# Performance work log

Hardware: AMD Instinct MI355X
Metric: run time of the kernel (lower is better)

Reference implementation:

```python
import jax, jax.numpy as jnp
import numpy as np

CLIP_LEN = 8      # == num_frame
NUM_NODES = 7     # == group_size
NUM_BASIC = 1024
NUM_MIXED = 8192
T = 2 * CLIP_LEN - 1          # 15 temporal offsets
N = 1 + NUM_NODES * CLIP_LEN  # 57 graph size


def setup_inputs() -> dict:
    key = jax.random.key(0)
    k1, k2, k3, k4 = jax.random.split(key, 4)
    mat = jax.random.normal(k1, (NUM_BASIC, NUM_NODES, NUM_NODES), dtype=jnp.float32)
    temp_extent = jax.random.normal(k2, (NUM_BASIC, T), dtype=jnp.float32)
    # nn.Linear(num_basic, num_mixed): weight [out,in], bias [out]
    W = jax.random.normal(k3, (NUM_MIXED, NUM_BASIC), dtype=jnp.float32) * (1.0 / np.sqrt(NUM_BASIC))
    b = jax.random.normal(k4, (NUM_MIXED,), dtype=jnp.float32) * 0.01
    return {"mat": mat, "temp_extent": temp_extent, "W": W, "b": b}


def reference(mat, temp_extent, W, b):
    n, cl = NUM_NODES, CLIP_LEN
    Hb = mat.shape[0]
    te = jax.nn.sigmoid(temp_extent) + 1.0                      # [Hb, T]
    x = jnp.einsum('ht,hnm->htmn', te, mat)                     # [Hb, T, n, n]
    x = jax.nn.relu(x)
    x = jnp.transpose(x, (1, 2, 3, 0)).reshape(T * n, n, Hb)    # (t m) n h
    y = x @ W.T + b                                             # [(t m), n, Hm]
    y = jax.nn.relu(jnp.transpose(y, (2, 1, 0)))                # [Hm, n, T*n]
    Hm = y.shape[0]
    # vectorized version of the per-frame slice-write loop:
    # frame i reads cols n*(cl-1-i) : n*(2*cl-1-i) of y
    starts = n * (cl - 1 - jnp.arange(cl))                      # [cl]
    idx = starts[:, None] + jnp.arange(n * cl)[None, :]         # [cl, n*cl]
    blocks = y[:, :, idx]                                       # [Hm, n, cl, n*cl]
    blocks = jnp.transpose(blocks, (0, 2, 1, 3)).reshape(Hm, n * cl, n * cl)
    base = jnp.zeros((Hm, N, N), dtype=y.dtype)
    base = base.at[:, 0::7, 0::7].set(1.0)                      # person-node anchors
    mixed = base.at[:, 1:, 1:].set(blocks)                      # [Hm, N, N]
    # degree normalization D^{-1/2} A D^{-1/2} (row sums, clamped at 1)
    d = jnp.clip(mixed.sum(axis=2), 1.0, None) ** -0.5          # [Hm, N]
    ret = d[:, :, None] * mixed * d[:, None, :]
    return ret
```

## Files before the change

kernel.cpp:

```cpp
#include <hip/hip_runtime.h>

#define HB 1024
#define HM 8192
#define NR 735
#define NPAD 768
#define NOUT 57

#define BM 64
#define BN 128
#define BK 64

typedef __attribute__((ext_vector_type(8))) _Float16 half8;
typedef __attribute__((ext_vector_type(4))) _Float16 half4v;
typedef __attribute__((ext_vector_type(4))) float floatx4;

__global__ __launch_bounds__(256) void prep_kernel(
    const float* __restrict__ mat, const float* __restrict__ tex,
    const float4* __restrict__ W,
    _Float16* __restrict__ Xh, half4v* __restrict__ Wh) {
  const int blk = blockIdx.x;
  if (blk < NPAD) {
    const int r = blk;
    const int n = r % 7;
    const int tm = r / 7;
    const int m = tm % 7;
    const int t = tm / 7;
#pragma unroll
    for (int i = 0; i < 4; ++i) {
      const int h = i * 256 + threadIdx.x;
      float v = 0.f;
      if (r < NR) {
        const float mv = mat[h * 49 + n * 7 + m];
        const float te = 1.f / (1.f + expf(-tex[h * 15 + t])) + 1.f;
        v = te * mv;
        v = v > 0.f ? v : 0.f;
      }
      Xh[r * HB + h] = (_Float16)v;
    }
  } else {
    const int idx = (blk - NPAD) * 256 + threadIdx.x;
    const float4 v = W[idx];
    half4v h;
    h.x = (_Float16)v.x;
    h.y = (_Float16)v.y;
    h.z = (_Float16)v.z;
    h.w = (_Float16)v.w;
    Wh[idx] = h;
  }
}

#define STAGE(pp, k0)                                                          \
  do {                                                                         \
    _Pragma("unroll")                                                          \
    for (int it_ = 0; it_ < 2; ++it_) {                                        \
      const int c_ = wave * 2 + it_;                                           \
      const int row_ = ((c_ & 3) * 16) + srow;                                 \
      const int kof_ = ((c_ >> 2) * 32) + skh;                                 \
      __builtin_amdgcn_global_load_lds(                                        \
          (const __attribute__((address_space(1))) void*)(                     \
              A + abase + (size_t)row_ * HB + (k0) + kof_),                    \
          (__attribute__((address_space(3))) void*)(&As[pp][c_ * 512 + lane * 8]), \
          16, 0, 0);                                                           \
    }                                                                          \
    _Pragma("unroll")                                                          \
    for (int it_ = 0; it_ < 4; ++it_) {                                        \
      const int c_ = wave * 4 + it_;                                           \
      const int row_ = ((c_ & 7) * 16) + srow;                                 \
      const int kof_ = ((c_ >> 3) * 32) + skh;                                 \
      __builtin_amdgcn_global_load_lds(                                        \
          (const __attribute__((address_space(1))) void*)(                     \
              B + bbase + (size_t)row_ * HB + (k0) + kof_),                    \
          (__attribute__((address_space(3))) void*)(&Bs[pp][c_ * 512 + lane * 8]), \
          16, 0, 0);                                                           \
    }                                                                          \
  } while (0)

__global__ __launch_bounds__(256) void gemm_kernel(
    const _Float16* __restrict__ A,
    const _Float16* __restrict__ B,
    const float* __restrict__ bias,
    float* __restrict__ Y) {
  __shared__ __align__(16) _Float16 As[2][BM * BK];
  __shared__ __align__(16) _Float16 Bs[2][BN * BK];

  const int tid = threadIdx.x;
  const int lane = tid & 63;
  const int wave = tid >> 6;

  const int bid = blockIdx.x;
  const int wg = (bid & 7) * 96 + (bid >> 3);
  const int bn = wg % 6;
  const int bm = wg / 6;

  const int wm = (wave >> 1) * 32;
  const int wn = (wave & 1) * 64;

  floatx4 acc[2][4] = {};

  const int srow = lane >> 2;
  const int skh = (lane & 3) * 8;
  const size_t abase = (size_t)(bm * BM) * HB;
  const size_t bbase = (size_t)(bn * BN) * HB;

  const int mrow = lane & 15;
  const int quad = lane >> 4;

  STAGE(0, 0);
  __syncthreads();

  int p = 0;
  for (int k0 = 0; k0 < HB; k0 += BK) {
    if (k0 + BK < HB) STAGE(p ^ 1, k0 + BK);

    half8 af[2][2], bf[2][4];
#pragma unroll
    for (int s = 0; s < 2; ++s) {
#pragma unroll
      for (int i = 0; i < 2; ++i)
        af[s][i] =
            *(const half8*)(&As[p][s * 2048 + (wm + i * 16 + mrow) * 32 + quad * 8]);
#pragma unroll
      for (int j = 0; j < 4; ++j)
        bf[s][j] =
            *(const half8*)(&Bs[p][s * 4096 + (wn + j * 16 + mrow) * 32 + quad * 8]);
    }
#pragma unroll
    for (int s = 0; s < 2; ++s)
#pragma unroll
      for (int i = 0; i < 2; ++i)
#pragma unroll
        for (int j = 0; j < 4; ++j)
          acc[i][j] = __builtin_amdgcn_mfma_f32_16x16x32_f16(af[s][i], bf[s][j],
                                                             acc[i][j], 0, 0, 0);

    __syncthreads();
    p ^= 1;
  }

#pragma unroll
  for (int i = 0; i < 2; ++i) {
#pragma unroll
    for (int j = 0; j < 4; ++j) {
#pragma unroll
      for (int reg = 0; reg < 4; ++reg) {
        const int grow = bm * BM + wm + i * 16 + quad * 4 + reg;
        const int gcol = bn * BN + wn + j * 16 + mrow;
        float v = acc[i][j][reg] + bias[grow];
        v = v > 0.f ? v : 0.f;
        Y[(size_t)grow * NPAD + gcol] = v;
      }
    }
  }
}

__global__ __launch_bounds__(256) void epilogue_kernel(
    const float* __restrict__ Y, float* __restrict__ out) {
  const int j0 = blockIdx.x * 4;
  __shared__ float ly[4][NR];
  __shared__ float dd[4][NOUT];

#pragma unroll
  for (int jj = 0; jj < 4; ++jj)
    for (int i = threadIdx.x; i < NR; i += 256)
      ly[jj][i] = Y[(size_t)(j0 + jj) * NPAD + i];
  __syncthreads();

  if (threadIdx.x < 4 * NOUT) {
    const int jj = threadIdx.x / NOUT;
    const int r = threadIdx.x % NOUT;
    float s;
    if (r == 0) {
      s = 9.f;
    } else {
      const int c = (r - 1) / 7;
      const int n = (r - 1) % 7;
      const int base = 7 * (7 - c);
      s = (n == 6) ? 1.f : 0.f;
      const float* lyj = ly[jj];
#pragma unroll
      for (int q = 0; q < 56; ++q) s += lyj[(base + q) * 7 + n];
    }
    s = s < 1.f ? 1.f : s;
    dd[jj][r] = rsqrtf(s);
  }
  __syncthreads();

  float4* ob = (float4*)(out + (size_t)j0 * (NOUT * NOUT));
  for (int v4 = threadIdx.x; v4 < NOUT * NOUT; v4 += 256) {
    float4 o;
#pragma unroll
    for (int e = 0; e < 4; ++e) {
      const int f = v4 * 4 + e;
      const int jj = f / (NOUT * NOUT);
      const int rem = f - jj * (NOUT * NOUT);
      const int r = rem / NOUT;
      const int q = rem - r * NOUT;
      const float* lyj = ly[jj];
      const float* dj = dd[jj];
      float val;
      if (r == 0) {
        val = (q % 7 == 0) ? dj[0] * dj[q] : 0.f;
      } else {
        const int c = (r - 1) / 7;
        const int n = (r - 1) % 7;
        if (q == 0)
          val = (n == 6) ? dj[r] * dj[0] : 0.f;
        else
          val = dj[r] * lyj[(7 * (7 - c) + q - 1) * 7 + n] * dj[q];
      }
      (&o.x)[e] = val;
    }
    ob[v4] = o;
  }
}

extern "C" void kernel_launch(void* const* d_in, const int* in_sizes, int n_in,
                              void* d_out, int out_size, void* d_ws, size_t ws_size,
                              hipStream_t stream) {
  const float* mat = (const float*)d_in[0];
  const float* tex = (const float*)d_in[1];
  const float* W = (const float*)d_in[2];
  const float* b = (const float*)d_in[3];
  float* out = (float*)d_out;

  char* ws = (char*)d_ws;
  _Float16* Xh = (_Float16*)(ws);
  _Float16* Wh = (_Float16*)(ws + (size_t)NPAD * HB * 2);
  float* Y = (float*)(ws + (size_t)NPAD * HB * 2 + (size_t)HM * HB * 2);

  prep_kernel<<<NPAD + HM * HB / 4 / 256, 256, 0, stream>>>(
      mat, tex, (const float4*)W, Xh, (half4v*)Wh);
  gemm_kernel<<<HM / BM * (NPAD / BN), 256, 0, stream>>>(Wh, Xh, b, Y);
  epilogue_kernel<<<HM / 4, 256, 0, stream>>>(Y, out);
}
```

Measured before the change: 187.1 us.

## Load GEMM fragments directly from global into registers, dropping LDS staging

The GEMM main loop no longer stages A and B tiles through LDS with global_load_lds and barriers. Each wave now reads its MFMA fragments straight from global memory into registers, using a two-set register double buffer that loads the next k-slice while the current one is multiplied. This removes the LDS traffic and __syncthreads, in exchange for redundant global/L2 reads, since waves sharing rows or columns each fetch their own copy. The last iteration issues a harmless wrap-around prefetch at k=0.

```diff
diff --git a/kernel.cpp b/kernel.cpp
--- a/kernel.cpp
+++ b/kernel.cpp
@@ -8,7 +8,6 @@
 
 #define BM 64
 #define BN 128
-#define BK 64
 
 typedef __attribute__((ext_vector_type(8))) _Float16 half8;
 typedef __attribute__((ext_vector_type(4))) _Float16 half4v;
@@ -49,30 +48,31 @@
   }
 }
 
-#define STAGE(pp, k0)                                                          \
-  do {                                                                         \
-    _Pragma("unroll")                                                          \
-    for (int it_ = 0; it_ < 2; ++it_) {                                        \
-      const int c_ = wave * 2 + it_;                                           \
-      const int row_ = ((c_ & 3) * 16) + srow;                                 \
-      const int kof_ = ((c_ >> 2) * 32) + skh;                                 \
-      __builtin_amdgcn_global_load_lds(                                        \
-          (const __attribute__((address_space(1))) void*)(                     \
-              A + abase + (size_t)row_ * HB + (k0) + kof_),                    \
-          (__attribute__((address_space(3))) void*)(&As[pp][c_ * 512 + lane * 8]), \
-          16, 0, 0);                                                           \
-    }                                                                          \
-    _Pragma("unroll")                                                          \
-    for (int it_ = 0; it_ < 4; ++it_) {                                        \
-      const int c_ = wave * 4 + it_;                                           \
-      const int row_ = ((c_ & 7) * 16) + srow;                                 \
-      const int kof_ = ((c_ >> 3) * 32) + skh;                                 \
-      __builtin_amdgcn_global_load_lds(                                        \
-          (const __attribute__((address_space(1))) void*)(                     \
-              B + bbase + (size_t)row_ * HB + (k0) + kof_),                    \
-          (__attribute__((address_space(3))) void*)(&Bs[pp][c_ * 512 + lane * 8]), \
-          16, 0, 0);                                                           \
-    }                                                                          \
+#define LOADF(af, bf, k0)                                                     \
+  do {                                                                        \
+    _Pragma("unroll")                                                         \
+    for (int s_ = 0; s_ < 2; ++s_) {                                          \
+      _Pragma("unroll")                                                       \
+      for (int i_ = 0; i_ < 2; ++i_)                                          \
+        af[s_][i_] =                                                          \
+            *(const half8*)(Abase + (size_t)i_ * 16 * HB + (k0) + s_ * 32);   \
+      _Pragma("unroll")                                                       \
+      for (int j_ = 0; j_ < 4; ++j_)                                          \
+        bf[s_][j_] =                                                          \
+            *(const half8*)(Bbase + (size_t)j_ * 16 * HB + (k0) + s_ * 32);   \
+    }                                                                         \
+  } while (0)
+
+#define MFMAS(af, bf)                                                         \
+  do {                                                                        \
+    _Pragma("unroll")                                                         \
+    for (int s_ = 0; s_ < 2; ++s_)                                            \
+      _Pragma("unroll")                                                       \
+      for (int i_ = 0; i_ < 2; ++i_)                                          \
+        _Pragma("unroll")                                                     \
+        for (int j_ = 0; j_ < 4; ++j_)                                        \
+          acc[i_][j_] = __builtin_amdgcn_mfma_f32_16x16x32_f16(               \
+              af[s_][i_], bf[s_][j_], acc[i_][j_], 0, 0, 0);                  \
   } while (0)
 
 __global__ __launch_bounds__(256) void gemm_kernel(
@@ -80,9 +80,6 @@
     const _Float16* __restrict__ B,
     const float* __restrict__ bias,
     float* __restrict__ Y) {
-  __shared__ __align__(16) _Float16 As[2][BM * BK];
-  __shared__ __align__(16) _Float16 Bs[2][BN * BK];
-
   const int tid = threadIdx.x;
   const int lane = tid & 63;
   const int wave = tid >> 6;
@@ -95,46 +92,23 @@
   const int wm = (wave >> 1) * 32;
   const int wn = (wave & 1) * 64;
 
-  floatx4 acc[2][4] = {};
-
-  const int srow = lane >> 2;
-  const int skh = (lane & 3) * 8;
-  const size_t abase = (size_t)(bm * BM) * HB;
-  const size_t bbase = (size_t)(bn * BN) * HB;
-
   const int mrow = lane & 15;
   const int quad = lane >> 4;
 
-  STAGE(0, 0);
-  __syncthreads();
-
-  int p = 0;
-  for (int k0 = 0; k0 < HB; k0 += BK) {
-    if (k0 + BK < HB) STAGE(p ^ 1, k0 + BK);
-
-    half8 af[2][2], bf[2][4];
-#pragma unroll
-    for (int s = 0; s < 2; ++s) {
-#pragma unroll
-      for (int i = 0; i < 2; ++i)
-        af[s][i] =
-            *(const half8*)(&As[p][s * 2048 + (wm + i * 16 + mrow) * 32 + quad * 8]);
-#pragma unroll
-      for (int j = 0; j < 4; ++j)
-        bf[s][j] =
-            *(const half8*)(&Bs[p][s * 4096 + (wn + j * 16 + mrow) * 32 + quad * 8]);
-    }
-#pragma unroll
-    for (int s = 0; s < 2; ++s)
-#pragma unroll
-      for (int i = 0; i < 2; ++i)
-#pragma unroll
-        for (int j = 0; j < 4; ++j)
-          acc[i][j] = __builtin_amdgcn_mfma_f32_16x16x32_f16(af[s][i], bf[s][j],
-                                                             acc[i][j], 0, 0, 0);
-
-    __syncthreads();
-    p ^= 1;
+  const _Float16* Abase = A + (size_t)(bm * BM + wm + mrow) * HB + quad * 8;
+  const _Float16* Bbase = B + (size_t)(bn * BN + wn + mrow) * HB + quad * 8;
+
+  floatx4 acc[2][4] = {};
+  half8 a0[2][2], b0[2][4], a1[2][2], b1[2][4];
+
+  LOADF(a0, b0, 0);
+#pragma unroll 1
+  for (int k0 = 0; k0 < HB; k0 += 128) {
+    LOADF(a1, b1, k0 + 64);
+    MFMAS(a0, b0);
+    const int kn = (k0 + 128 < HB) ? k0 + 128 : 0;
+    LOADF(a0, b0, kn);
+    MFMAS(a1, b1);
   }
 
 #pragma unroll
```

Result: slower. 234.2 us (+25.2%).

## Fuse fp32-to-fp16 weight conversion into GEMM A-tile loading

Applied to the files above, without the earlier changes.

Drops the separate pass that converted the full weight matrix to fp16 in the workspace. The GEMM now reads fp32 weights directly through registers, converts them, and writes them to LDS while the MFMAs for the current tile run. BK is halved to 32 to keep the register-staged A path and the LDS footprint manageable. This saves a full write and re-read of the 16 MB fp16 weight copy. The cost is that each of the 6 column blocks re-reads the fp32 weights at twice the bytes, and the K loop runs twice as many iterations with more barriers.

```diff
diff --git a/kernel.cpp b/kernel.cpp
--- a/kernel.cpp
+++ b/kernel.cpp
@@ -8,75 +8,57 @@
 
 #define BM 64
 #define BN 128
-#define BK 64
+#define BK 32
 
 typedef __attribute__((ext_vector_type(8))) _Float16 half8;
-typedef __attribute__((ext_vector_type(4))) _Float16 half4v;
 typedef __attribute__((ext_vector_type(4))) float floatx4;
 
 __global__ __launch_bounds__(256) void prep_kernel(
     const float* __restrict__ mat, const float* __restrict__ tex,
-    const float4* __restrict__ W,
-    _Float16* __restrict__ Xh, half4v* __restrict__ Wh) {
-  const int blk = blockIdx.x;
-  if (blk < NPAD) {
-    const int r = blk;
-    const int n = r % 7;
-    const int tm = r / 7;
-    const int m = tm % 7;
-    const int t = tm / 7;
-#pragma unroll
-    for (int i = 0; i < 4; ++i) {
-      const int h = i * 256 + threadIdx.x;
-      float v = 0.f;
-      if (r < NR) {
-        const float mv = mat[h * 49 + n * 7 + m];
-        const float te = 1.f / (1.f + expf(-tex[h * 15 + t])) + 1.f;
-        v = te * mv;
-        v = v > 0.f ? v : 0.f;
-      }
-      Xh[r * HB + h] = (_Float16)v;
-    }
-  } else {
-    const int idx = (blk - NPAD) * 256 + threadIdx.x;
-    const float4 v = W[idx];
-    half4v h;
-    h.x = (_Float16)v.x;
-    h.y = (_Float16)v.y;
-    h.z = (_Float16)v.z;
-    h.w = (_Float16)v.w;
-    Wh[idx] = h;
-  }
-}
-
-#define STAGE(pp, k0)                                                          \
+    _Float16* __restrict__ Xh) {
+  const int r = blockIdx.x;
+  const int n = r % 7;
+  const int tm = r / 7;
+  const int m = tm % 7;
+  const int t = tm / 7;
+#pragma unroll
+  for (int i = 0; i < 4; ++i) {
+    const int h = i * 256 + threadIdx.x;
+    float v = 0.f;
+    if (r < NR) {
+      const float mv = mat[h * 49 + n * 7 + m];
+      const float te = 1.f / (1.f + expf(-tex[h * 15 + t])) + 1.f;
+      v = te * mv;
+      v = v > 0.f ? v : 0.f;
+    }
+    Xh[r * HB + h] = (_Float16)v;
+  }
+}
+
+#define STAGE_B(pp, k0)                                                        \
   do {                                                                         \
     _Pragma("unroll")                                                          \
     for (int it_ = 0; it_ < 2; ++it_) {                                        \
       const int c_ = wave * 2 + it_;                                           \
-      const int row_ = ((c_ & 3) * 16) + srow;                                 \
-      const int kof_ = ((c_ >> 2) * 32) + skh;                                 \
+      const int row_ = c_ * 16 + srow;                                         \
       __builtin_amdgcn_global_load_lds(                                        \
           (const __attribute__((address_space(1))) void*)(                     \
-              A + abase + (size_t)row_ * HB + (k0) + kof_),                    \
-          (__attribute__((address_space(3))) void*)(&As[pp][c_ * 512 + lane * 8]), \
-          16, 0, 0);                                                           \
-    }                                                                          \
-    _Pragma("unroll")                                                          \
-    for (int it_ = 0; it_ < 4; ++it_) {                                        \
-      const int c_ = wave * 4 + it_;                                           \
-      const int row_ = ((c_ & 7) * 16) + srow;                                 \
-      const int kof_ = ((c_ >> 3) * 32) + skh;                                 \
-      __builtin_amdgcn_global_load_lds(                                        \
-          (const __attribute__((address_space(1))) void*)(                     \
-              B + bbase + (size_t)row_ * HB + (k0) + kof_),                    \
-          (__attribute__((address_space(3))) void*)(&Bs[pp][c_ * 512 + lane * 8]), \
+              B + bbase + (size_t)row_ * HB + (k0) + skh),                     \
+          (__attribute__((address_space(3))) void*)(&Bs[pp][c_ * 512]),        \
           16, 0, 0);                                                           \
     }                                                                          \
   } while (0)
 
+#define CVT8(h, r0, r1)                                                        \
+  do {                                                                         \
+    h[0] = (_Float16)r0.x; h[1] = (_Float16)r0.y;                              \
+    h[2] = (_Float16)r0.z; h[3] = (_Float16)r0.w;                              \
+    h[4] = (_Float16)r1.x; h[5] = (_Float16)r1.y;                              \
+    h[6] = (_Float16)r1.z; h[7] = (_Float16)r1.w;                              \
+  } while (0)
+
 __global__ __launch_bounds__(256) void gemm_kernel(
-    const _Float16* __restrict__ A,
+    const float* __restrict__ W,
     const _Float16* __restrict__ B,
     const float* __restrict__ bias,
     float* __restrict__ Y) {
@@ -97,42 +79,57 @@
 
   floatx4 acc[2][4] = {};
 
+  const int arow = wave * 16 + (lane >> 2);
+  const int akh = (lane & 3) * 8;
+  const float* Ap = W + (size_t)(bm * BM + arow) * HB + akh;
+  const int alds = arow * BK + akh;
+
   const int srow = lane >> 2;
   const int skh = (lane & 3) * 8;
-  const size_t abase = (size_t)(bm * BM) * HB;
   const size_t bbase = (size_t)(bn * BN) * HB;
 
   const int mrow = lane & 15;
   const int quad = lane >> 4;
 
-  STAGE(0, 0);
+  {
+    float4 r0 = *(const float4*)(Ap + 0);
+    float4 r1 = *(const float4*)(Ap + 4);
+    half8 h;
+    CVT8(h, r0, r1);
+    *(half8*)(&As[0][alds]) = h;
+  }
+  STAGE_B(0, 0);
   __syncthreads();
 
   int p = 0;
   for (int k0 = 0; k0 < HB; k0 += BK) {
-    if (k0 + BK < HB) STAGE(p ^ 1, k0 + BK);
-
-    half8 af[2][2], bf[2][4];
-#pragma unroll
-    for (int s = 0; s < 2; ++s) {
-#pragma unroll
-      for (int i = 0; i < 2; ++i)
-        af[s][i] =
-            *(const half8*)(&As[p][s * 2048 + (wm + i * 16 + mrow) * 32 + quad * 8]);
+    const int next = k0 + BK;
+    float4 r0, r1;
+    if (next < HB) {
+      r0 = *(const float4*)(Ap + next);
+      r1 = *(const float4*)(Ap + next + 4);
+      STAGE_B(p ^ 1, next);
+    }
+
+    half8 af[2], bf[4];
+#pragma unroll
+    for (int i = 0; i < 2; ++i)
+      af[i] = *(const half8*)(&As[p][(wm + i * 16 + mrow) * BK + quad * 8]);
+#pragma unroll
+    for (int j = 0; j < 4; ++j)
+      bf[j] = *(const half8*)(&Bs[p][(wn + j * 16 + mrow) * BK + quad * 8]);
+#pragma unroll
+    for (int i = 0; i < 2; ++i)
 #pragma unroll
       for (int j = 0; j < 4; ++j)
-        bf[s][j] =
-            *(const half8*)(&Bs[p][s * 4096 + (wn + j * 16 + mrow) * 32 + quad * 8]);
-    }
-#pragma unroll
-    for (int s = 0; s < 2; ++s)
-#pragma unroll
-      for (int i = 0; i < 2; ++i)
-#pragma unroll
-        for (int j = 0; j < 4; ++j)
-          acc[i][j] = __builtin_amdgcn_mfma_f32_16x16x32_f16(af[s][i], bf[s][j],
-                                                             acc[i][j], 0, 0, 0);
-
+        acc[i][j] =
+            __builtin_amdgcn_mfma_f32_16x16x32_f16(af[i], bf[j], acc[i][j], 0, 0, 0);
+
+    if (next < HB) {
+      half8 h;
+      CVT8(h, r0, r1);
+      *(half8*)(&As[p ^ 1][alds]) = h;
+    }
     __syncthreads();
     p ^= 1;
   }
@@ -225,11 +222,9 @@
 
   char* ws = (char*)d_ws;
   _Float16* Xh = (_Float16*)(ws);
-  _Float16* Wh = (_Float16*)(ws + (size_t)NPAD * HB * 2);
-  float* Y = (float*)(ws + (size_t)NPAD * HB * 2 + (size_t)HM * HB * 2);
-
-  prep_kernel<<<NPAD + HM * HB / 4 / 256, 256, 0, stream>>>(
-      mat, tex, (const float4*)W, Xh, (half4v*)Wh);
-  gemm_kernel<<<HM / BM * (NPAD / BN), 256, 0, stream>>>(Wh, Xh, b, Y);
+  float* Y = (float*)(ws + (size_t)NPAD * HB * 2);
+
+  prep_kernel<<<NPAD, 256, 0, stream>>>(mat, tex, Xh);
+  gemm_kernel<<<HM / BM * (NPAD / BN), 256, 0, stream>>>(W, Xh, b, Y);
   epilogue_kernel<<<HM / 4, 256, 0, stream>>>(Y, out);
 }
```

Measured after the change: 196.9 us. +5.3%, slower.

## Triple-buffer GEMM LDS stages with BK 32 and one barrier per step

Applied to the files above, without the earlier changes.

The GEMM K-tile shrinks from 64 to 32 and the two LDS buffers become three. Loads run two stages ahead, and each iteration waits with vmcnt so that only the current stage must have landed. A single raw s_barrier per iteration replaces the trailing __syncthreads, so global-to-LDS loads can overlap MFMA work across iterations. In exchange there are twice as many loop iterations and fewer MFMAs per barrier, and correctness depends on hand-counted vmcnt values.

```diff
diff --git a/kernel.cpp b/kernel.cpp
--- a/kernel.cpp
+++ b/kernel.cpp
@@ -8,7 +8,7 @@
 
 #define BM 64
 #define BN 128
-#define BK 64
+#define BK 32
 
 typedef __attribute__((ext_vector_type(8))) _Float16 half8;
 typedef __attribute__((ext_vector_type(4))) _Float16 half4v;
@@ -51,28 +51,39 @@
 
 #define STAGE(pp, k0)                                                          \
   do {                                                                         \
+    const int arow_ = wave * 16 + srow;                                        \
+    __builtin_amdgcn_global_load_lds(                                          \
+        (const __attribute__((address_space(1))) void*)(                       \
+            A + abase + (size_t)arow_ * HB + (k0) + skh),                      \
+        (__attribute__((address_space(3))) void*)(&As[pp][wave * 512]),        \
+        16, 0, 0);                                                             \
     _Pragma("unroll")                                                          \
     for (int it_ = 0; it_ < 2; ++it_) {                                        \
       const int c_ = wave * 2 + it_;                                           \
-      const int row_ = ((c_ & 3) * 16) + srow;                                 \
-      const int kof_ = ((c_ >> 2) * 32) + skh;                                 \
+      const int brow_ = c_ * 16 + srow;                                        \
       __builtin_amdgcn_global_load_lds(                                        \
           (const __attribute__((address_space(1))) void*)(                     \
-              A + abase + (size_t)row_ * HB + (k0) + kof_),                    \
-          (__attribute__((address_space(3))) void*)(&As[pp][c_ * 512 + lane * 8]), \
+              B + bbase + (size_t)brow_ * HB + (k0) + skh),                    \
+          (__attribute__((address_space(3))) void*)(&Bs[pp][c_ * 512]),        \
           16, 0, 0);                                                           \
     }                                                                          \
-    _Pragma("unroll")                                                          \
-    for (int it_ = 0; it_ < 4; ++it_) {                                        \
-      const int c_ = wave * 4 + it_;                                           \
-      const int row_ = ((c_ & 7) * 16) + srow;                                 \
-      const int kof_ = ((c_ >> 3) * 32) + skh;                                 \
-      __builtin_amdgcn_global_load_lds(                                        \
-          (const __attribute__((address_space(1))) void*)(                     \
-              B + bbase + (size_t)row_ * HB + (k0) + kof_),                    \
-          (__attribute__((address_space(3))) void*)(&Bs[pp][c_ * 512 + lane * 8]), \
-          16, 0, 0);                                                           \
-    }                                                                          \
+  } while (0)
+
+#define COMPUTE(pp)                                                            \
+  do {                                                                         \
+    half8 af[2], bf[4];                                                        \
+    _Pragma("unroll")                                                          \
+    for (int i_ = 0; i_ < 2; ++i_)                                             \
+      af[i_] = *(const half8*)(&As[pp][(wm + i_ * 16 + mrow) * BK + quad * 8]);\
+    _Pragma("unroll")                                                          \
+    for (int j_ = 0; j_ < 4; ++j_)                                             \
+      bf[j_] = *(const half8*)(&Bs[pp][(wn + j_ * 16 + mrow) * BK + quad * 8]);\
+    _Pragma("unroll")                                                          \
+    for (int i_ = 0; i_ < 2; ++i_)                                             \
+      _Pragma("unroll")                                                        \
+      for (int j_ = 0; j_ < 4; ++j_)                                           \
+        acc[i_][j_] = __builtin_amdgcn_mfma_f32_16x16x32_f16(                  \
+            af[i_], bf[j_], acc[i_][j_], 0, 0, 0);                             \
   } while (0)
 
 __global__ __launch_bounds__(256) void gemm_kernel(
@@ -80,8 +91,8 @@
     const _Float16* __restrict__ B,
     const float* __restrict__ bias,
     float* __restrict__ Y) {
-  __shared__ __align__(16) _Float16 As[2][BM * BK];
-  __shared__ __align__(16) _Float16 Bs[2][BN * BK];
+  __shared__ __align__(16) _Float16 As[3][BM * BK];
+  __shared__ __align__(16) _Float16 Bs[3][BN * BK];
 
   const int tid = threadIdx.x;
   const int lane = tid & 63;
@@ -106,36 +117,28 @@
   const int quad = lane >> 4;
 
   STAGE(0, 0);
-  __syncthreads();
+  STAGE(1, BK);
 
   int p = 0;
-  for (int k0 = 0; k0 < HB; k0 += BK) {
-    if (k0 + BK < HB) STAGE(p ^ 1, k0 + BK);
-
-    half8 af[2][2], bf[2][4];
-#pragma unroll
-    for (int s = 0; s < 2; ++s) {
-#pragma unroll
-      for (int i = 0; i < 2; ++i)
-        af[s][i] =
-            *(const half8*)(&As[p][s * 2048 + (wm + i * 16 + mrow) * 32 + quad * 8]);
-#pragma unroll
-      for (int j = 0; j < 4; ++j)
-        bf[s][j] =
-            *(const half8*)(&Bs[p][s * 4096 + (wn + j * 16 + mrow) * 32 + quad * 8]);
-    }
-#pragma unroll
-    for (int s = 0; s < 2; ++s)
-#pragma unroll
-      for (int i = 0; i < 2; ++i)
-#pragma unroll
-        for (int j = 0; j < 4; ++j)
-          acc[i][j] = __builtin_amdgcn_mfma_f32_16x16x32_f16(af[s][i], bf[s][j],
-                                                             acc[i][j], 0, 0, 0);
-
-    __syncthreads();
-    p ^= 1;
-  }
+#pragma unroll 1
+  for (int k0 = 0; k0 < HB - BK; k0 += BK) {
+    asm volatile("s_waitcnt vmcnt(3)" ::: "memory");
+    __builtin_amdgcn_sched_barrier(0);
+    __builtin_amdgcn_s_barrier();
+    __builtin_amdgcn_sched_barrier(0);
+
+    const int pn = (p + 2 >= 3) ? p - 1 : p + 2;
+    if (k0 + 2 * BK < HB) STAGE(pn, k0 + 2 * BK);
+
+    COMPUTE(p);
+    p = (p == 2) ? 0 : p + 1;
+  }
+
+  asm volatile("s_waitcnt vmcnt(0)" ::: "memory");
+  __builtin_amdgcn_sched_barrier(0);
+  __builtin_amdgcn_s_barrier();
+  __builtin_amdgcn_sched_barrier(0);
+  COMPUTE(p);
 
 #pragma unroll
   for (int i = 0; i < 2; ++i) {
```

Measured after the change: 188.8 us. Within noise of the previous version (+0.9%).
